# Kernel tuning notes

Hardware: AMD Instinct MI355X
Metric: run time of the kernel (lower is better)

The kernel has to match this reference:

```python
import jax, jax.numpy as jnp
import numpy as np
from jax import lax

NUM_LAYERS = 4
EPS_BN = 1e-5
EPS_AGG = 1e-6


def _bn(x, gamma, beta):
    # training-mode batch norm over the leading (node/edge) dim
    m = x.mean(axis=0)
    v = x.var(axis=0)
    return gamma * (x - m) / jnp.sqrt(v + EPS_BN) + beta


def setup_inputs() -> dict:
    key = jax.random.key(0)
    ks = jax.random.split(key, 32)
    N, E, D, L, K = 50000, 400000, 64, 128, 16
    s = 0.05
    inp = {
        'reads': jax.random.uniform(ks[0], (N, 4, L), jnp.float32),
        'src': jax.random.randint(ks[1], (E,), 0, N, jnp.int32),
        'dst': jax.random.randint(ks[2], (E,), 0, N, jnp.int32),
        'overlap_similarity': jax.random.uniform(ks[3], (E,), jnp.float32),
        'overlap_length': jax.random.normal(ks[4], (E,), jnp.float32),
        # sequence encoder conv: Conv1d(4 -> D, kernel K)
        'conv_w': jax.random.normal(ks[5], (D, 4, K), jnp.float32) * s,
        'conv_b': jnp.zeros((D,), jnp.float32),
        # edge encoder: Linear(2 -> D)
        'We': jax.random.normal(ks[6], (2, D), jnp.float32) * s,
        'be': jnp.zeros((D,), jnp.float32),
        # GatedGCN per-layer weights, stacked on leading layer dim
        'A1': jax.random.normal(ks[7], (NUM_LAYERS, D, D), jnp.float32) * s,
        'A2': jax.random.normal(ks[8], (NUM_LAYERS, D, D), jnp.float32) * s,
        'A3': jax.random.normal(ks[9], (NUM_LAYERS, D, D), jnp.float32) * s,
        'bA1': jnp.zeros((NUM_LAYERS, D), jnp.float32),
        'bA2': jnp.zeros((NUM_LAYERS, D), jnp.float32),
        'bA3': jnp.zeros((NUM_LAYERS, D), jnp.float32),
        'U': jax.random.normal(ks[10], (NUM_LAYERS, D, D), jnp.float32) * s,
        'V': jax.random.normal(ks[11], (NUM_LAYERS, D, D), jnp.float32) * s,
        'bU': jnp.zeros((NUM_LAYERS, D), jnp.float32),
        'bV': jnp.zeros((NUM_LAYERS, D), jnp.float32),
        'bn_h_gamma': jnp.ones((NUM_LAYERS, D), jnp.float32),
        'bn_h_beta': jnp.zeros((NUM_LAYERS, D), jnp.float32),
        'bn_e_gamma': jnp.ones((NUM_LAYERS, D), jnp.float32),
        'bn_e_beta': jnp.zeros((NUM_LAYERS, D), jnp.float32),
        # edge decoder MLP: Linear(3D -> D) -> ReLU -> Linear(D -> 1)
        'W1': jax.random.normal(ks[12], (3 * D, D), jnp.float32) * s,
        'b1': jnp.zeros((D,), jnp.float32),
        'W2': jax.random.normal(ks[13], (D, 1), jnp.float32) * s,
        'b2': jnp.zeros((1,), jnp.float32),
    }
    return inp


def reference(reads, src, dst, overlap_similarity, overlap_length,
              conv_w, conv_b, We, be,
              A1, A2, A3, bA1, bA2, bA3, U, V, bU, bV,
              bn_h_gamma, bn_h_beta, bn_e_gamma, bn_e_beta,
              W1, b1, W2, b2):
    N = reads.shape[0]
    # --- SequenceEncoder: Conv1d over one-hot reads, global max-pool ---
    hseq = lax.conv_general_dilated(
        reads, conv_w, window_strides=(1,), padding='VALID',
        dimension_numbers=('NCH', 'OIH', 'NCH'))  # [N, D, L-K+1]
    h = (hseq + conv_b[None, :, None]).max(axis=2)  # [N, D]
    # --- EdgeEncoder: Linear on [similarity, length] ---
    e = jnp.stack([overlap_similarity, overlap_length], axis=1) @ We + be  # [E, D]
    # --- stacked GatedGCN layers (gather src/dst, scatter-aggregate to dst) ---
    for l in range(NUM_LAYERS):
        hs = h[src]  # [E, D] gather
        hd = h[dst]
        e_hat = (hs @ A1[l] + bA1[l]) + (hd @ A2[l] + bA2[l]) + (e @ A3[l] + bA3[l])
        sigma = jax.nn.sigmoid(e_hat)  # edge gates
        Vh = hs @ V[l] + bV[l]
        num = jax.ops.segment_sum(sigma * Vh, dst, num_segments=N)  # [N, D]
        den = jax.ops.segment_sum(sigma, dst, num_segments=N)
        h_hat = (h @ U[l] + bU[l]) + num / (den + EPS_AGG)
        h = h + jax.nn.relu(_bn(h_hat, bn_h_gamma[l], bn_h_beta[l]))
        e = e + jax.nn.relu(_bn(e_hat, bn_e_gamma[l], bn_e_beta[l]))
    # --- EdgeDecoder: MLP on [h_src, h_dst, e] ---
    z = jnp.concatenate([h[src], h[dst], e], axis=1)  # [E, 3D]
    p = jax.nn.relu(z @ W1 + b1) @ W2 + b2  # [E, 1]
    return p
```

## Files before the change

### kernel.cpp

```cpp
#include <hip/hip_runtime.h>
#include <hip/hip_bf16.h>
#include <cstdint>
#include <cstddef>

#define DD 64

typedef __attribute__((ext_vector_type(8))) short short8;
typedef __attribute__((ext_vector_type(4))) float f32x4;

__device__ __forceinline__ float4 f4_0() { return make_float4(0.f, 0.f, 0.f, 0.f); }

__device__ __forceinline__ unsigned short f2bf(float f) {
  __hip_bfloat16 h = __float2bfloat16(f);
  return *reinterpret_cast<unsigned short*>(&h);
}
__device__ __forceinline__ float bfl(unsigned u) { return __uint_as_float(u << 16); }
__device__ __forceinline__ float bfh(unsigned u) { return __uint_as_float(u & 0xffff0000u); }
__device__ __forceinline__ float b2f(unsigned short u) {
  return __uint_as_float(((unsigned)u) << 16);
}

__device__ __forceinline__ short8 pack_bf16x8(float4 a, float4 b) {
  union { unsigned short us[8]; short8 v; } pk;
  pk.us[0] = f2bf(a.x); pk.us[1] = f2bf(a.y); pk.us[2] = f2bf(a.z); pk.us[3] = f2bf(a.w);
  pk.us[4] = f2bf(b.x); pk.us[5] = f2bf(b.y); pk.us[6] = f2bf(b.z); pk.us[7] = f2bf(b.w);
  return pk.v;
}

__device__ __forceinline__ short8 lds_frag(const unsigned short* p) {
  uint2 lo = *reinterpret_cast<const uint2*>(p);
  uint2 hi = *reinterpret_cast<const uint2*>(p + 4);
  union { unsigned u[4]; short8 v; } t;
  t.u[0] = lo.x; t.u[1] = lo.y; t.u[2] = hi.x; t.u[3] = hi.y;
  return t.v;
}
__device__ __forceinline__ short8 g_frag(const unsigned short* p) {
  return *reinterpret_cast<const short8*>(p);
}

__global__ __launch_bounds__(256) void k_hist(const int* __restrict__ dst,
                                              int* __restrict__ cnt, int E) {
  int j = blockIdx.x * 256 + threadIdx.x;
  if (j < E) atomicAdd(&cnt[dst[j]], 1);
}

__global__ __launch_bounds__(1024) void k_scan(const int* __restrict__ cnt,
                                               int* __restrict__ row_ptr,
                                               int* __restrict__ nxt, int N, int E) {
  __shared__ int wsum[16];
  __shared__ int carry_s;
  const int tid = threadIdx.x;
  const int wid = tid >> 6, lane = tid & 63;
  if (tid == 0) carry_s = 0;
  __syncthreads();
  const int ntl = (N + 4095) / 4096;
  for (int b = 0; b < ntl; ++b) {
    const int i0 = b * 4096 + tid * 4;
    int v0 = 0, v1 = 0, v2 = 0, v3 = 0;
    if (i0 + 3 < N) {
      int4 q = *reinterpret_cast<const int4*>(cnt + i0);
      v0 = q.x; v1 = q.y; v2 = q.z; v3 = q.w;
    } else {
      if (i0 < N) v0 = cnt[i0];
      if (i0 + 1 < N) v1 = cnt[i0 + 1];
      if (i0 + 2 < N) v2 = cnt[i0 + 2];
      if (i0 + 3 < N) v3 = cnt[i0 + 3];
    }
    const int tsum = v0 + v1 + v2 + v3;
    int x = tsum;
#pragma unroll
    for (int off = 1; off < 64; off <<= 1) {
      int y = __shfl_up(x, off, 64);
      if (lane >= off) x += y;
    }
    if (lane == 63) wsum[wid] = x;
    __syncthreads();
    if (wid == 0 && lane < 16) {
      int wv = wsum[lane];
#pragma unroll
      for (int off = 1; off < 16; off <<= 1) {
        int y = __shfl_up(wv, off, 64);
        if (lane >= off) wv += y;
      }
      wsum[lane] = wv;
    }
    __syncthreads();
    int base = carry_s + (wid > 0 ? wsum[wid - 1] : 0) + (x - tsum);
    int e1 = base + v0, e2 = e1 + v1, e3 = e2 + v2;
    if (i0 < N) { row_ptr[i0] = base; nxt[i0] = base; }
    if (i0 + 1 < N) { row_ptr[i0 + 1] = e1; nxt[i0 + 1] = e1; }
    if (i0 + 2 < N) { row_ptr[i0 + 2] = e2; nxt[i0 + 2] = e2; }
    if (i0 + 3 < N) { row_ptr[i0 + 3] = e3; nxt[i0 + 3] = e3; }
    __syncthreads();
    if (tid == 0) carry_s += wsum[15];
    __syncthreads();
  }
  if (tid == 0) row_ptr[N] = E;
}

__global__ __launch_bounds__(256) void k_scatter(const int* __restrict__ dst,
                                                 const int* __restrict__ src,
                                                 int* __restrict__ nxt,
                                                 int* __restrict__ order,
                                                 int* __restrict__ psrc,
                                                 int* __restrict__ pdst, int E) {
  int j = blockIdx.x * 256 + threadIdx.x;
  if (j >= E) return;
  int d = dst[j];
  int pos = atomicAdd(&nxt[d], 1);
  order[pos] = j;
  psrc[pos] = src[j];
  pdst[pos] = d;
}

__global__ __launch_bounds__(256) void k_prep(const float* __restrict__ A1,
                                              const float* __restrict__ A2,
                                              const float* __restrict__ V,
                                              const float* __restrict__ U,
                                              const float* __restrict__ A3,
                                              const float* __restrict__ W1,
                                              unsigned short* __restrict__ T) {
  const int b = blockIdx.x;
  const int tid = threadIdx.x;
  if (b < 20) {
    const int l = b / 5, m = b % 5;
    const float* srcp =
        (m == 0 ? A1 : m == 1 ? A2 : m == 2 ? V : m == 3 ? U : A3) + l * 4096;
    unsigned short* dstp = T + b * 4096;
    for (int i = tid; i < 4096; i += 256) {
      int n = i >> 6, k = i & 63;
      dstp[i] = f2bf(srcp[k * 64 + n]);
    }
  } else {
    unsigned short* dstp = T + 20 * 4096;
    for (int i = tid; i < 12288; i += 256) {
      int n = i / 192, k = i % 192;
      dstp[i] = f2bf(W1[k * 64 + n]);
    }
  }
}

struct ConvRegs { float4 v[3][2]; };

__device__ __forceinline__ void conv_load(const float* __restrict__ reads, int N,
                                          int g, int tid, ConvRegs& R) {
#pragma unroll
  for (int it = 0; it < 3; ++it) {
    const int task = tid + it * 256;
    R.v[it][0] = f4_0(); R.v[it][1] = f4_0();
    if (task < 576) {
      const int node = task / 144, rem = task % 144;
      const int c = rem / 36, u = rem % 36;
      const int gn = g * 4 + node;
      if (gn < N) {
        const float* rp = reads + (size_t)gn * 512 + c * 128 + 4 * u;
        if (u <= 31) R.v[it][0] = *reinterpret_cast<const float4*>(rp);
        if (u <= 30) R.v[it][1] = *reinterpret_cast<const float4*>(rp + 4);
      }
    }
  }
}

__device__ __forceinline__ void conv_write(unsigned short* __restrict__ cbuf,
                                           int tid, const ConvRegs& R) {
#pragma unroll
  for (int it = 0; it < 3; ++it) {
    const int task = tid + it * 256;
    if (task < 576) {
      const int node = task / 144, rem = task % 144;
      const int c = rem / 36, u = rem % 36;
      const float4 v0 = R.v[it][0], v1 = R.v[it][1];
      unsigned pk0, pk1, pk2, pk3;
      asm("v_cvt_pk_bf16_f32 %0, %1, %2" : "=v"(pk0) : "v"(v0.x), "v"(v0.y));
      asm("v_cvt_pk_bf16_f32 %0, %1, %2" : "=v"(pk1) : "v"(v0.z), "v"(v0.w));
      asm("v_cvt_pk_bf16_f32 %0, %1, %2" : "=v"(pk2) : "v"(v1.x), "v"(v1.y));
      asm("v_cvt_pk_bf16_f32 %0, %1, %2" : "=v"(pk3) : "v"(v1.z), "v"(v1.w));
      const unsigned a0 = __builtin_amdgcn_alignbit(pk1, pk0, 16);
      const unsigned a1 = __builtin_amdgcn_alignbit(pk2, pk1, 16);
      const unsigned a2 = __builtin_amdgcn_alignbit(pk3, pk2, 16);
      const int base = ((node * 4 + c) * 4) * 144 + 4 * u;
      *reinterpret_cast<uint2*>(&cbuf[base + 0 * 144]) = make_uint2(pk0, pk1);
      *reinterpret_cast<uint2*>(&cbuf[base + 1 * 144]) = make_uint2(a0, a1);
      *reinterpret_cast<uint2*>(&cbuf[base + 2 * 144]) = make_uint2(pk1, pk2);
      *reinterpret_cast<uint2*>(&cbuf[base + 3 * 144]) = make_uint2(a1, a2);
    }
  }
}

__global__ __launch_bounds__(256) void k_conv_mfma(const float* __restrict__ reads,
                                                   const float* __restrict__ w,
                                                   const float* __restrict__ bias,
                                                   float* __restrict__ h, int N) {
  __shared__ unsigned short cp[2][4 * 4 * 4 * 144];
  const int tid = threadIdx.x;
  const int wid = tid >> 6, lane = tid & 63;
// ... 105 lines not shown
  }
  const int wid = tid >> 6, lane = tid & 63;
  const int col = lane & 15, g = lane >> 4;
  const int ntiles = (N + 15) / 16;
  for (int tw = blockIdx.x * 4 + wid; tw < ntiles; tw += gridDim.x * 4) {
    int n = tw * 16 + col;
    const bool valid = n < N;
    if (!valid) n = N - 1;
    short8 bfr[2];
#pragma unroll
    for (int ks = 0; ks < 2; ++ks) {
      const int c0 = ks * 32 + g * 8;
      const float* hp = h_in + (size_t)n * 64 + c0;
      float4 x0 = *reinterpret_cast<const float4*>(hp);
      float4 x1 = *reinterpret_cast<const float4*>(hp + 4);
      if (hasupd) {
        const float* yp = hhat + (size_t)n * 64 + c0;
        float4 y0 = *reinterpret_cast<const float4*>(yp);
        float4 y1 = *reinterpret_cast<const float4*>(yp + 4);
        float4 sc0 = *reinterpret_cast<const float4*>(&s_coef[c0]);
        float4 sc1 = *reinterpret_cast<const float4*>(&s_coef[c0 + 4]);
        float4 sh0 = *reinterpret_cast<const float4*>(&s_coef[64 + c0]);
        float4 sh1 = *reinterpret_cast<const float4*>(&s_coef[64 + c0 + 4]);
        x0.x += fmaxf(fmaf(sc0.x, y0.x, sh0.x), 0.f);
        x0.y += fmaxf(fmaf(sc0.y, y0.y, sh0.y), 0.f);
        x0.z += fmaxf(fmaf(sc0.z, y0.z, sh0.z), 0.f);
        x0.w += fmaxf(fmaf(sc0.w, y0.w, sh0.w), 0.f);
        x1.x += fmaxf(fmaf(sc1.x, y1.x, sh1.x), 0.f);
        x1.y += fmaxf(fmaf(sc1.y, y1.y, sh1.y), 0.f);
        x1.z += fmaxf(fmaf(sc1.z, y1.z, sh1.z), 0.f);
        x1.w += fmaxf(fmaf(sc1.w, y1.w, sh1.w), 0.f);
        if (valid) {
          float* op = h_out + (size_t)n * 64 + c0;
          *reinterpret_cast<float4*>(op) = x0;
          *reinterpret_cast<float4*>(op + 4) = x1;
        }
      }
      bfr[ks] = pack_bf16x8(x0, x1);
    }
#pragma unroll
    for (int m = 0; m < 4; ++m) {
      const unsigned short* Wm = Wt4 + m * 4096;
      f32x4 acc[4] = {};
#pragma unroll
      for (int ks = 0; ks < 2; ++ks) {
        const int ko = ks * 32 + g * 8;
#pragma unroll
        for (int mt = 0; mt < 4; ++mt) {
          short8 aa = g_frag(Wm + (mt * 16 + col) * 64 + ko);
          acc[mt] = __builtin_amdgcn_mfma_f32_16x16x32_bf16(aa, bfr[ks], acc[mt], 0, 0, 0);
        }
      }
      if (!valid) continue;
      const float* bb = (m == 0) ? bA1 : (m == 1) ? bA2 : (m == 2) ? bV : bU;
#pragma unroll
      for (int mt = 0; mt < 4; ++mt) {
        const int chb = mt * 16 + g * 4;
        float4 bv = *reinterpret_cast<const float4*>(bb + chb);
        float o0 = acc[mt][0] + bv.x;
        float o1 = acc[mt][1] + bv.y;
        float o2 = acc[mt][2] + bv.z;
        float o3 = acc[mt][3] + bv.w;
        if (m < 3) {
          unsigned short* X = (m == 0) ? XA1 : (m == 1) ? XA2 : XV;
          ushort4 ov;
          ov.x = f2bf(o0); ov.y = f2bf(o1); ov.z = f2bf(o2); ov.w = f2bf(o3);
          *reinterpret_cast<ushort4*>(X + (size_t)n * 64 + chb) = ov;
        } else {
          *reinterpret_cast<float4*>(XU + (size_t)n * 64 + chb) =
              make_float4(o0, o1, o2, o3);
        }
      }
    }
  }
}

__global__ __launch_bounds__(256) void k_edge_mfma0(unsigned short* __restrict__ e,
                                                    unsigned short* __restrict__ ehat_out,
                                                    const float* __restrict__ sim,
                                                    const float* __restrict__ olen,
                                                    const int* __restrict__ order,
                                                    const float* __restrict__ We,
                                                    const float* __restrict__ be,
                                                    const int* __restrict__ psrc,
                                                    const int* __restrict__ pdst,
                                                    const unsigned short* __restrict__ XA1,
                                                    const unsigned short* __restrict__ XA2,
                                                    const unsigned short* __restrict__ A3t,
                                                    const float* __restrict__ bA3,
                                                    float* __restrict__ sums_out, int E) {
  __shared__ float s_sums[128];
  const int tid = threadIdx.x;
  if (tid < 128) s_sums[tid] = 0.f;
  __syncthreads();
  const int wid = tid >> 6, lane = tid & 63;
  const int col = lane & 15, g = lane >> 4;
  short8 aa[4][2];
#pragma unroll
  for (int mt = 0; mt < 4; ++mt)
#pragma unroll
    for (int ks = 0; ks < 2; ++ks)
      aa[mt][ks] = g_frag(A3t + (mt * 16 + col) * 64 + ks * 32 + g * 8);
  float4 ba[4];
#pragma unroll
  for (int mt = 0; mt < 4; ++mt)
    ba[mt] = *reinterpret_cast<const float4*>(bA3 + mt * 16 + g * 4);
  float4 w0[2][2], w1[2][2], bev[2][2];
#pragma unroll
  for (int ks = 0; ks < 2; ++ks) {
    const int c0 = ks * 32 + g * 8;
    w0[ks][0] = *reinterpret_cast<const float4*>(We + c0);
    w0[ks][1] = *reinterpret_cast<const float4*>(We + c0 + 4);
    w1[ks][0] = *reinterpret_cast<const float4*>(We + 64 + c0);
    w1[ks][1] = *reinterpret_cast<const float4*>(We + 64 + c0 + 4);
    bev[ks][0] = *reinterpret_cast<const float4*>(be + c0);
    bev[ks][1] = *reinterpret_cast<const float4*>(be + c0 + 4);
  }
  float statS[16], statQ[16];
#pragma unroll
  for (int i = 0; i < 16; ++i) { statS[i] = 0.f; statQ[i] = 0.f; }
  const int ntiles = (E + 15) / 16;
  for (int tw = blockIdx.x * 4 + wid; tw < ntiles; tw += gridDim.x * 4) {
    int p = tw * 16 + col;
    const bool valid = p < E;
    if (!valid) p = E - 1;
    const int se = psrc[p], de = pdst[p];
    const int oe = order[p];
    const float sv = sim[oe], lv = olen[oe];
    short8 bfr[2];
#pragma unroll
    for (int ks = 0; ks < 2; ++ks) {
      float4 e0, e1;
      e0.x = fmaf(sv, w0[ks][0].x, fmaf(lv, w1[ks][0].x, bev[ks][0].x));
      e0.y = fmaf(sv, w0[ks][0].y, fmaf(lv, w1[ks][0].y, bev[ks][0].y));
      e0.z = fmaf(sv, w0[ks][0].z, fmaf(lv, w1[ks][0].z, bev[ks][0].z));
      e0.w = fmaf(sv, w0[ks][0].w, fmaf(lv, w1[ks][0].w, bev[ks][0].w));
      e1.x = fmaf(sv, w0[ks][1].x, fmaf(lv, w1[ks][1].x, bev[ks][1].x));
      e1.y = fmaf(sv, w0[ks][1].y, fmaf(lv, w1[ks][1].y, bev[ks][1].y));
      e1.z = fmaf(sv, w0[ks][1].z, fmaf(lv, w1[ks][1].z, bev[ks][1].z));
      e1.w = fmaf(sv, w0[ks][1].w, fmaf(lv, w1[ks][1].w, bev[ks][1].w));
      bfr[ks] = pack_bf16x8(e0, e1);
      if (valid)
        *reinterpret_cast<short8*>(e + (size_t)p * 64 + ks * 32 + g * 8) = bfr[ks];
    }
    f32x4 acc[4] = {};
#pragma unroll
    for (int ks = 0; ks < 2; ++ks)
#pragma unroll
      for (int mt = 0; mt < 4; ++mt)
        acc[mt] = __builtin_amdgcn_mfma_f32_16x16x32_bf16(aa[mt][ks], bfr[ks], acc[mt], 0, 0, 0);
    if (valid) {
#pragma unroll
      for (int mt = 0; mt < 4; ++mt) {
        const int chb = mt * 16 + g * 4;
        ushort4 x1 = *reinterpret_cast<const ushort4*>(XA1 + (size_t)se * 64 + chb);
        ushort4 x2 = *reinterpret_cast<const ushort4*>(XA2 + (size_t)de * 64 + chb);
        float o0 = acc[mt][0] + b2f(x1.x) + b2f(x2.x) + ba[mt].x;
        float o1 = acc[mt][1] + b2f(x1.y) + b2f(x2.y) + ba[mt].y;
        float o2 = acc[mt][2] + b2f(x1.z) + b2f(x2.z) + ba[mt].z;
        float o3 = acc[mt][3] + b2f(x1.w) + b2f(x2.w) + ba[mt].w;
        ushort4 ov;
        ov.x = f2bf(o0); ov.y = f2bf(o1); ov.z = f2bf(o2); ov.w = f2bf(o3);
        *reinterpret_cast<ushort4*>(ehat_out + (size_t)p * 64 + chb) = ov;
        statS[mt * 4 + 0] += o0; statQ[mt * 4 + 0] = fmaf(o0, o0, statQ[mt * 4 + 0]);
        statS[mt * 4 + 1] += o1; statQ[mt * 4 + 1] = fmaf(o1, o1, statQ[mt * 4 + 1]);
        statS[mt * 4 + 2] += o2; statQ[mt * 4 + 2] = fmaf(o2, o2, statQ[mt * 4 + 2]);
        statS[mt * 4 + 3] += o3; statQ[mt * 4 + 3] = fmaf(o3, o3, statQ[mt * 4 + 3]);
      }
    }
  }
#pragma unroll
  for (int off = 1; off <= 8; off <<= 1)
#pragma unroll
    for (int i = 0; i < 16; ++i) {
      statS[i] += __shfl_xor(statS[i], off, 64);
      statQ[i] += __shfl_xor(statQ[i], off, 64);
    }
  if (col == 0) {
#pragma unroll
    for (int mt = 0; mt < 4; ++mt)
#pragma unroll
      for (int c = 0; c < 4; ++c) {
        const int ch = mt * 16 + g * 4 + c;
        atomicAdd(&s_sums[ch], statS[mt * 4 + c]);
        atomicAdd(&s_sums[64 + ch], statQ[mt * 4 + c]);
      }
  }
  __syncthreads();
  if (tid < 128) atomicAdd(&sums_out[tid], s_sums[tid]);
}

__global__ __launch_bounds__(256) void k_edge_mfma(unsigned short* __restrict__ e,
                                                   const unsigned short* __restrict__ ehat_prev,
                                                   unsigned short* __restrict__ ehat_out,
                                                   const float* __restrict__ sums_prev,
                                                   const float* __restrict__ gprev,
                                                   const float* __restrict__ bprev,
                                                   const int* __restrict__ psrc,
                                                   const int* __restrict__ pdst,
                                                   const unsigned short* __restrict__ XA1,
                                                   const unsigned short* __restrict__ XA2,
                                                   const unsigned short* __restrict__ A3t,
                                                   const float* __restrict__ bA3,
                                                   float* __restrict__ sums_out, int E) {
  __shared__ float s_coef[128];
  __shared__ float s_sums[128];
  const int tid = threadIdx.x;
  if (tid < 128) s_sums[tid] = 0.f;
  if (tid < 64) {
    float mean = sums_prev[tid] / (float)E;
    float var = sums_prev[64 + tid] / (float)E - mean * mean;
    float sc = gprev[tid] * rsqrtf(var + 1e-5f);
    s_coef[tid] = sc;
    s_coef[64 + tid] = bprev[tid] - mean * sc;
  }
  __syncthreads();
  const int wid = tid >> 6, lane = tid & 63;
  const int col = lane & 15, g = lane >> 4;
  short8 aa[4][2];
#pragma unroll
  for (int mt = 0; mt < 4; ++mt)
#pragma unroll
    for (int ks = 0; ks < 2; ++ks)
      aa[mt][ks] = g_frag(A3t + (mt * 16 + col) * 64 + ks * 32 + g * 8);
  float4 ba[4];
#pragma unroll
  for (int mt = 0; mt < 4; ++mt)
    ba[mt] = *reinterpret_cast<const float4*>(bA3 + mt * 16 + g * 4);
  float statS[16], statQ[16];
#pragma unroll
  for (int i = 0; i < 16; ++i) { statS[i] = 0.f; statQ[i] = 0.f; }
  const int ntiles = (E + 15) / 16;
  for (int tw = blockIdx.x * 4 + wid; tw < ntiles; tw += gridDim.x * 4) {
    int p = tw * 16 + col;
    const bool valid = p < E;
    if (!valid) p = E - 1;
    const int se = psrc[p], de = pdst[p];
    short8 bfr[2];
#pragma unroll
    for (int ks = 0; ks < 2; ++ks) {
      const int c0 = ks * 32 + g * 8;
      uint4 eo = *reinterpret_cast<const uint4*>(e + (size_t)p * 64 + c0);
      float4 e0 = make_float4(bfl(eo.x), bfh(eo.x), bfl(eo.y), bfh(eo.y));
      float4 e1 = make_float4(bfl(eo.z), bfh(eo.z), bfl(eo.w), bfh(eo.w));
      uint4 hv = *reinterpret_cast<const uint4*>(ehat_prev + (size_t)p * 64 + c0);
      float4 sc0 = *reinterpret_cast<const float4*>(&s_coef[c0]);
      float4 sc1 = *reinterpret_cast<const float4*>(&s_coef[c0 + 4]);
      float4 sh0 = *reinterpret_cast<const float4*>(&s_coef[64 + c0]);
      float4 sh1 = *reinterpret_cast<const float4*>(&s_coef[64 + c0 + 4]);
      e0.x += fmaxf(fmaf(sc0.x, bfl(hv.x), sh0.x), 0.f);
      e0.y += fmaxf(fmaf(sc0.y, bfh(hv.x), sh0.y), 0.f);
      e0.z += fmaxf(fmaf(sc0.z, bfl(hv.y), sh0.z), 0.f);
      e0.w += fmaxf(fmaf(sc0.w, bfh(hv.y), sh0.w), 0.f);
      e1.x += fmaxf(fmaf(sc1.x, bfl(hv.z), sh1.x), 0.f);
      e1.y += fmaxf(fmaf(sc1.y, bfh(hv.z), sh1.y), 0.f);
      e1.z += fmaxf(fmaf(sc1.z, bfl(hv.w), sh1.z), 0.f);
      e1.w += fmaxf(fmaf(sc1.w, bfh(hv.w), sh1.w), 0.f);
      bfr[ks] = pack_bf16x8(e0, e1);
      if (valid)
        *reinterpret_cast<short8*>(e + (size_t)p * 64 + c0) = bfr[ks];
    }
    f32x4 acc[4] = {};
#pragma unroll
    for (int ks = 0; ks < 2; ++ks)
#pragma unroll
      for (int mt = 0; mt < 4; ++mt)
        acc[mt] = __builtin_amdgcn_mfma_f32_16x16x32_bf16(aa[mt][ks], bfr[ks], acc[mt], 0, 0, 0);
    if (valid) {
#pragma unroll
      for (int mt = 0; mt < 4; ++mt) {
        const int chb = mt * 16 + g * 4;
        ushort4 x1 = *reinterpret_cast<const ushort4*>(XA1 + (size_t)se * 64 + chb);
        ushort4 x2 = *reinterpret_cast<const ushort4*>(XA2 + (size_t)de * 64 + chb);
        float o0 = acc[mt][0] + b2f(x1.x) + b2f(x2.x) + ba[mt].x;
        float o1 = acc[mt][1] + b2f(x1.y) + b2f(x2.y) + ba[mt].y;
        float o2 = acc[mt][2] + b2f(x1.z) + b2f(x2.z) + ba[mt].z;
        float o3 = acc[mt][3] + b2f(x1.w) + b2f(x2.w) + ba[mt].w;
        ushort4 ov;
        ov.x = f2bf(o0); ov.y = f2bf(o1); ov.z = f2bf(o2); ov.w = f2bf(o3);
        *reinterpret_cast<ushort4*>(ehat_out + (size_t)p * 64 + chb) = ov;
        statS[mt * 4 + 0] += o0; statQ[mt * 4 + 0] = fmaf(o0, o0, statQ[mt * 4 + 0]);
        statS[mt * 4 + 1] += o1; statQ[mt * 4 + 1] = fmaf(o1, o1, statQ[mt * 4 + 1]);
        statS[mt * 4 + 2] += o2; statQ[mt * 4 + 2] = fmaf(o2, o2, statQ[mt * 4 + 2]);
        statS[mt * 4 + 3] += o3; statQ[mt * 4 + 3] = fmaf(o3, o3, statQ[mt * 4 + 3]);
      }
    }
  }
#pragma unroll
  for (int off = 1; off <= 8; off <<= 1)
#pragma unroll
    for (int i = 0; i < 16; ++i) {
      statS[i] += __shfl_xor(statS[i], off, 64);
      statQ[i] += __shfl_xor(statQ[i], off, 64);
    }
  if (col == 0) {
#pragma unroll
    for (int mt = 0; mt < 4; ++mt)
#pragma unroll
      for (int c = 0; c < 4; ++c) {
        const int ch = mt * 16 + g * 4 + c;
        atomicAdd(&s_sums[ch], statS[mt * 4 + c]);
        atomicAdd(&s_sums[64 + ch], statQ[mt * 4 + c]);
      }
  }
  __syncthreads();
  if (tid < 128) atomicAdd(&sums_out[tid], s_sums[tid]);
}

__global__ __launch_bounds__(256) void k_agg(const int* __restrict__ row_ptr,
                                             const int* __restrict__ psrc,
                                             const unsigned short* __restrict__ ehat,
                                             const unsigned short* __restrict__ XV,
                                             const float* __restrict__ XU,
                                             float* __restrict__ hhat,
                                             float* __restrict__ sums_h, int N) {
  __shared__ float s_sums[128];
  const int tid = threadIdx.x;
  if (tid < 128) s_sums[tid] = 0.f;
  __syncthreads();
  float sS[4] = {0.f, 0.f, 0.f, 0.f}, sQ[4] = {0.f, 0.f, 0.f, 0.f};
  const int total = N * 16;
  for (int idx = blockIdx.x * 256 + tid; idx < total; idx += gridDim.x * 256) {
    int n = idx >> 4, dc = (idx & 15) << 2;
    int beg = row_ptr[n], end = row_ptr[n + 1];
    float4 nm = f4_0(), dn = f4_0();
    for (int i = beg; i < end; ++i) {
      int sj = psrc[i];
      uint2 ev = *reinterpret_cast<const uint2*>(ehat + (size_t)i * 64 + dc);
      uint2 vv = *reinterpret_cast<const uint2*>(XV + (size_t)sj * 64 + dc);
      float s0 = 1.f / (1.f + __expf(-bfl(ev.x)));
      float s1 = 1.f / (1.f + __expf(-bfh(ev.x)));
      float s2 = 1.f / (1.f + __expf(-bfl(ev.y)));
      float s3 = 1.f / (1.f + __expf(-bfh(ev.y)));
      dn.x += s0; dn.y += s1; dn.z += s2; dn.w += s3;
      nm.x = fmaf(s0, bfl(vv.x), nm.x);
      nm.y = fmaf(s1, bfh(vv.x), nm.y);
      nm.z = fmaf(s2, bfl(vv.y), nm.z);
      nm.w = fmaf(s3, bfh(vv.y), nm.w);
    }
    float4 xu = *reinterpret_cast<const float4*>(XU + (size_t)n * 64 + dc);
    float h0 = xu.x + nm.x / (dn.x + 1e-6f);
    float h1 = xu.y + nm.y / (dn.y + 1e-6f);
    float h2 = xu.z + nm.z / (dn.z + 1e-6f);
    float h3 = xu.w + nm.w / (dn.w + 1e-6f);
    *reinterpret_cast<float4*>(hhat + (size_t)n * 64 + dc) = make_float4(h0, h1, h2, h3);
    sS[0] += h0; sQ[0] = fmaf(h0, h0, sQ[0]);
    sS[1] += h1; sQ[1] = fmaf(h1, h1, sQ[1]);
    sS[2] += h2; sQ[2] = fmaf(h2, h2, sQ[2]);
    sS[3] += h3; sQ[3] = fmaf(h3, h3, sQ[3]);
  }
#pragma unroll
  for (int off = 16; off <= 32; off <<= 1)
#pragma unroll
    for (int c = 0; c < 4; ++c) {
      sS[c] += __shfl_xor(sS[c], off, 64);
      sQ[c] += __shfl_xor(sQ[c], off, 64);
    }
  const int lane = tid & 63;
  if (lane < 16) {
    const int dc = lane << 2;
#pragma unroll
    for (int c = 0; c < 4; ++c) {
      atomicAdd(&s_sums[dc + c], sS[c]);
      atomicAdd(&s_sums[64 + dc + c], sQ[c]);
    }
  }
  __syncthreads();
  if (tid < 128) atomicAdd(&sums_h[tid], s_sums[tid]);
}

__global__ __launch_bounds__(256) void k_update_h(float* __restrict__ h,
                                                  const float* __restrict__ hhat,
                                                  const float* __restrict__ sums,
                                                  const float* __restrict__ gamma,
                                                  const float* __restrict__ beta, int R) {
  int idx = blockIdx.x * 256 + threadIdx.x;
  if (idx >= R * 16) return;
  int r = idx >> 4, dc = (idx & 15) << 2;
  const float invR = 1.f / (float)R;
  float4 sv = *reinterpret_cast<const float4*>(sums + dc);
  float4 qv = *reinterpret_cast<const float4*>(sums + 64 + dc);
  float4 gm = *reinterpret_cast<const float4*>(gamma + dc);
  float4 bt = *reinterpret_cast<const float4*>(beta + dc);
  float m0 = sv.x * invR, m1 = sv.y * invR, m2 = sv.z * invR, m3 = sv.w * invR;
  float c0 = gm.x * rsqrtf(qv.x * invR - m0 * m0 + 1e-5f);
  float c1 = gm.y * rsqrtf(qv.y * invR - m1 * m1 + 1e-5f);
  float c2 = gm.z * rsqrtf(qv.z * invR - m2 * m2 + 1e-5f);
  float c3 = gm.w * rsqrtf(qv.w * invR - m3 * m3 + 1e-5f);
  float h0 = bt.x - m0 * c0, h1 = bt.y - m1 * c1, h2 = bt.z - m2 * c2, h3 = bt.w - m3 * c3;
  size_t off = (size_t)r * 64 + dc;
  float4 y = *reinterpret_cast<const float4*>(hhat + off);
  float4 x = *reinterpret_cast<const float4*>(h + off);
  x.x += fmaxf(fmaf(c0, y.x, h0), 0.f);
  x.y += fmaxf(fmaf(c1, y.y, h1), 0.f);
  x.z += fmaxf(fmaf(c2, y.z, h2), 0.f);
  x.w += fmaxf(fmaf(c3, y.w, h3), 0.f);
  *reinterpret_cast<float4*>(h + off) = x;
}

__global__ __launch_bounds__(256) void k_decoder_mfma(const float* __restrict__ h,
                                                      const unsigned short* __restrict__ e,
                                                      const unsigned short* __restrict__ ehat3,
                                                      const float* __restrict__ sums_e3,
                                                      const float* __restrict__ ge3,
                                                      const float* __restrict__ be3,
                                                      const int* __restrict__ psrc,
                                                      const int* __restrict__ pdst,
                                                      const int* __restrict__ order,
                                                      const unsigned short* __restrict__ W1t,
                                                      const float* __restrict__ b1,
                                                      const float* __restrict__ W2,
                                                      const float* __restrict__ b2,
                                                      float* __restrict__ out, int E) {
  __shared__ unsigned short Wt[64 * 200];
  __shared__ float s_coef[128];
  const int tid = threadIdx.x;
  if (tid < 64) {
    float mean = sums_e3[tid] / (float)E;
    float var = sums_e3[64 + tid] / (float)E - mean * mean;
    float sc = ge3[tid] * rsqrtf(var + 1e-5f);
    s_coef[tid] = sc;
    s_coef[64 + tid] = be3[tid] - mean * sc;
  }
  for (int i = tid; i < 1536; i += 256) {
    int n = i / 24, kc = (i % 24) * 8;
    *reinterpret_cast<uint4*>(&Wt[n * 200 + kc]) =
        *reinterpret_cast<const uint4*>(W1t + n * 192 + kc);
  }
  __syncthreads();
  const int wid = tid >> 6, lane = tid & 63;
  const int col = lane & 15, g = lane >> 4;
  float b1v[4], w2v[4];
#pragma unroll
  for (int nt = 0; nt < 4; ++nt) { b1v[nt] = b1[nt * 16 + col]; w2v[nt] = W2[nt * 16 + col]; }
  const float bb2 = b2[0];
  const int ntiles = (E + 15) / 16;
  for (int tw = blockIdx.x * 4 + wid; tw < ntiles; tw += gridDim.x * 4) {
    const int eb = tw * 16;
    int p = eb + col;
    if (p >= E) p = E - 1;
    const int se = psrc[p], de = pdst[p];
    f32x4 acc[4] = {};
#pragma unroll
    for (int ks = 0; ks < 6; ++ks) {
      float4 a0, a1;
      if (ks < 4) {
        const float* ap = (ks < 2 ? h + (size_t)se * 64 : h + (size_t)de * 64) + (ks & 1) * 32 + g * 8;
        a0 = *reinterpret_cast<const float4*>(ap);
        a1 = *reinterpret_cast<const float4*>(ap + 4);
      } else {
        const int c0 = (ks - 4) * 32 + g * 8;
        uint4 eo = *reinterpret_cast<const uint4*>(e + (size_t)p * 64 + c0);
        a0 = make_float4(bfl(eo.x), bfh(eo.x), bfl(eo.y), bfh(eo.y));
        a1 = make_float4(bfl(eo.z), bfh(eo.z), bfl(eo.w), bfh(eo.w));
        uint4 hv = *reinterpret_cast<const uint4*>(ehat3 + (size_t)p * 64 + c0);
        float4 sc0 = *reinterpret_cast<const float4*>(&s_coef[c0]);
        float4 sc1 = *reinterpret_cast<const float4*>(&s_coef[c0 + 4]);
        float4 sh0 = *reinterpret_cast<const float4*>(&s_coef[64 + c0]);
        float4 sh1 = *reinterpret_cast<const float4*>(&s_coef[64 + c0 + 4]);
        a0.x += fmaxf(fmaf(sc0.x, bfl(hv.x), sh0.x), 0.f);
        a0.y += fmaxf(fmaf(sc0.y, bfh(hv.x), sh0.y), 0.f);
        a0.z += fmaxf(fmaf(sc0.z, bfl(hv.y), sh0.z), 0.f);
        a0.w += fmaxf(fmaf(sc0.w, bfh(hv.y), sh0.w), 0.f);
        a1.x += fmaxf(fmaf(sc1.x, bfl(hv.z), sh1.x), 0.f);
        a1.y += fmaxf(fmaf(sc1.y, bfh(hv.z), sh1.y), 0.f);
        a1.z += fmaxf(fmaf(sc1.z, bfl(hv.w), sh1.z), 0.f);
        a1.w += fmaxf(fmaf(sc1.w, bfh(hv.w), sh1.w), 0.f);
      }
      short8 af = pack_bf16x8(a0, a1);
#pragma unroll
      for (int nt = 0; nt < 4; ++nt) {
        short8 bb = lds_frag(&Wt[(nt * 16 + col) * 200 + ks * 32 + g * 8]);
        acc[nt] = __builtin_amdgcn_mfma_f32_16x16x32_bf16(af, bb, acc[nt], 0, 0, 0);
      }
    }
    float pr[4];
#pragma unroll
    for (int r = 0; r < 4; ++r) {
      float s = 0.f;
#pragma unroll
      for (int nt = 0; nt < 4; ++nt)
        s = fmaf(fmaxf(acc[nt][r] + b1v[nt], 0.f), w2v[nt], s);
      pr[r] = s;
    }
#pragma unroll
    for (int off = 1; off <= 8; off <<= 1)
#pragma unroll
      for (int r = 0; r < 4; ++r)
        pr[r] += __shfl_xor(pr[r], off, 64);
    if (col == 0) {
#pragma unroll
      for (int r = 0; r < 4; ++r) {
        int m = eb + g * 4 + r;
        if (m < E) out[order[m]] = pr[r] + bb2;
      }
    }
  }
}

extern "C" void kernel_launch(void* const* d_in, const int* in_sizes, int n_in,
                              void* d_out, int out_size, void* d_ws, size_t ws_size,
                              hipStream_t stream) {
  const float* reads  = (const float*)d_in[0];
  const int*   src    = (const int*)d_in[1];
  const int*   dst    = (const int*)d_in[2];
  const float* sim    = (const float*)d_in[3];
  const float* olen   = (const float*)d_in[4];
  const float* conv_w = (const float*)d_in[5];
  const float* conv_b = (const float*)d_in[6];
  const float* We     = (const float*)d_in[7];
  const float* be     = (const float*)d_in[8];
  const float* A1     = (const float*)d_in[9];
  const float* A2     = (const float*)d_in[10];
  const float* A3     = (const float*)d_in[11];
  const float* bA1    = (const float*)d_in[12];
  const float* bA2    = (const float*)d_in[13];
  const float* bA3    = (const float*)d_in[14];
  const float* U      = (const float*)d_in[15];
  const float* V      = (const float*)d_in[16];
  const float* bU     = (const float*)d_in[17];
  const float* bV     = (const float*)d_in[18];
  const float* bnhg   = (const float*)d_in[19];
  const float* bnhb   = (const float*)d_in[20];
  const float* bneg   = (const float*)d_in[21];
  const float* bneb   = (const float*)d_in[22];
  const float* W1     = (const float*)d_in[23];
  const float* b1     = (const float*)d_in[24];
  const float* W2     = (const float*)d_in[25];
  const float* b2     = (const float*)d_in[26];

  const int N = in_sizes[0] / 512;
  const int E = in_sizes[1];

  float* fp = (float*)d_ws;
  float* hA   = fp; fp += (size_t)N * 64;
  float* hB   = fp; fp += (size_t)N * 64;
  float* hhat = fp; fp += (size_t)N * 64;
  float* XU   = fp; fp += (size_t)N * 64;
  float* sums = fp; fp += 1024;
  unsigned short* up = (unsigned short*)fp;
  unsigned short* e     = up; up += (size_t)E * 64;
  unsigned short* ehatA = up; up += (size_t)E * 64;
  unsigned short* ehatB = up; up += (size_t)E * 64;
  unsigned short* XA1 = up; up += (size_t)N * 64;
  unsigned short* XA2 = up; up += (size_t)N * 64;
  unsigned short* XV  = up; up += (size_t)N * 64;
  unsigned short* Wt  = up; up += 20 * 4096 + 12288;
  int* ip = (int*)up;
  int* order   = ip; ip += E;
  int* psrc    = ip; ip += E;
  int* pdst    = ip; ip += E;
  int* cnt     = ip; ip += N;
  int* nxt     = ip; ip += N;
  int* row_ptr = ip; ip += N + 1;
  float* out = (float*)d_out;

  hipMemsetAsync(cnt, 0, sizeof(int) * N, stream);
  hipMemsetAsync(sums, 0, sizeof(float) * 1024, stream);
  k_hist<<<(E + 255) / 256, 256, 0, stream>>>(dst, cnt, E);
  k_prep<<<21, 256, 0, stream>>>(A1, A2, V, U, A3, W1, Wt);
  k_scan<<<1, 1024, 0, stream>>>(cnt, row_ptr, nxt, N, E);
  k_scatter<<<(E + 255) / 256, 256, 0, stream>>>(dst, src, nxt, order, psrc, pdst, E);

  const int ngroups = (N + 3) / 4;
  const int CG = ngroups < 1024 ? ngroups : 1024;
  k_conv_mfma<<<CG, 256, 0, stream>>>(reads, conv_w, conv_b, hA, N);

  const int EPBLK = 2048;
  const int APBLK = 1024;
  const int NPB = 512;
  float* hin = hA;
  float* hout = hB;
  unsigned short* ehat_cur = ehatA;
  unsigned short* ehat_prev = ehatB;
  for (int l = 0; l < 4; ++l) {
    ehat_cur = (l & 1) ? ehatB : ehatA;
    ehat_prev = (l & 1) ? ehatA : ehatB;
    float* sums_e = sums + l * 128;
    float* sums_h = sums + 512 + l * 128;
    k_node_mfma<<<NPB, 256, 0, stream>>>(
        hin, (l > 0) ? hout : nullptr, hhat,
        (l > 0) ? (sums + 512 + (l - 1) * 128) : sums,
        bnhg + (l > 0 ? (l - 1) * 64 : 0), bnhb + (l > 0 ? (l - 1) * 64 : 0),
        Wt + l * 5 * 4096,
        bA1 + l * 64, bA2 + l * 64, bV + l * 64, bU + l * 64,
        XA1, XA2, XV, XU, N, l > 0 ? 1 : 0);
    if (l > 0) { float* t = hin; hin = hout; hout = t; }
    if (l == 0) {
      k_edge_mfma0<<<EPBLK, 256, 0, stream>>>(
          e, ehat_cur, sim, olen, order, We, be, psrc, pdst, XA1, XA2,
          Wt + 4 * 4096, bA3, sums_e, E);
    } else {
      k_edge_mfma<<<EPBLK, 256, 0, stream>>>(
          e, ehat_prev, ehat_cur, sums + (l - 1) * 128,
          bneg + (l - 1) * 64, bneb + (l - 1) * 64,
          psrc, pdst, XA1, XA2, Wt + (l * 5 + 4) * 4096, bA3 + l * 64, sums_e, E);
    }
    k_agg<<<APBLK, 256, 0, stream>>>(row_ptr, psrc, ehat_cur, XV, XU, hhat, sums_h, N);
  }

  k_update_h<<<(N * 16 + 255) / 256, 256, 0, stream>>>(
      hin, hhat, sums + 512 + 3 * 128, bnhg + 3 * 64, bnhb + 3 * 64, N);
  k_decoder_mfma<<<EPBLK, 256, 0, stream>>>(
      hin, e, ehat_cur, sums + 3 * 128, bneg + 3 * 64, bneb + 3 * 64,
      psrc, pdst, order, Wt + 20 * 4096, b1, W2, b2, out, E);
}
```

Measured before the change: 856.0 us.

## Prefetch next-tile edge data, pack src/dst pairs, bf16 decoder node features

The edge kernels now software-pipeline their grid-stride loop. Each iteration prefetches the next tile's packed (src,dst) int2 indices and its contiguous e/ehat rows, and issues the XA1/XA2 gathers before the MFMA so their latency overlaps compute. The A3 weight fragments are reloaded from global memory inside the loop instead of being held in registers, which frees registers for the prefetched data. The final h update also writes a bf16 copy of h, so the decoder gathers half the bytes and skips the float-to-bf16 packing for node features. The edge grid is halved to 1024 blocks, which lowers occupancy in exchange for longer per-wave loops and more register room.

```diff
diff --git a/kernel.cpp b/kernel.cpp
--- a/kernel.cpp
+++ b/kernel.cpp
@@ -36,6 +36,9 @@
 }
 __device__ __forceinline__ short8 g_frag(const unsigned short* p) {
   return *reinterpret_cast<const short8*>(p);
+}
+__device__ __forceinline__ short8 u4_to_s8(uint4 v) {
+  union { uint4 u; short8 s; } t; t.u = v; return t.s;
 }
 
 __global__ __launch_bounds__(256) void k_hist(const int* __restrict__ dst,
@@ -103,14 +106,15 @@
                                                  int* __restrict__ nxt,
                                                  int* __restrict__ order,
                                                  int* __restrict__ psrc,
-                                                 int* __restrict__ pdst, int E) {
+                                                 int2* __restrict__ pedge, int E) {
   int j = blockIdx.x * 256 + threadIdx.x;
   if (j >= E) return;
   int d = dst[j];
+  int s = src[j];
   int pos = atomicAdd(&nxt[d], 1);
   order[pos] = j;
-  psrc[pos] = src[j];
-  pdst[pos] = d;
+  psrc[pos] = s;
+  pedge[pos] = make_int2(s, d);
 }
 
 __global__ __launch_bounds__(256) void k_prep(const float* __restrict__ A1,
@@ -382,8 +386,7 @@
                                                     const int* __restrict__ order,
                                                     const float* __restrict__ We,
                                                     const float* __restrict__ be,
-                                                    const int* __restrict__ psrc,
-                                                    const int* __restrict__ pdst,
+                                                    const int2* __restrict__ pedge,
                                                     const unsigned short* __restrict__ XA1,
                                                     const unsigned short* __restrict__ XA2,
                                                     const unsigned short* __restrict__ A3t,
@@ -395,12 +398,6 @@
   __syncthreads();
   const int wid = tid >> 6, lane = tid & 63;
   const int col = lane & 15, g = lane >> 4;
-  short8 aa[4][2];
-#pragma unroll
-  for (int mt = 0; mt < 4; ++mt)
-#pragma unroll
-    for (int ks = 0; ks < 2; ++ks)
-      aa[mt][ks] = g_frag(A3t + (mt * 16 + col) * 64 + ks * 32 + g * 8);
   float4 ba[4];
 #pragma unroll
   for (int mt = 0; mt < 4; ++mt)
@@ -420,13 +417,34 @@
 #pragma unroll
   for (int i = 0; i < 16; ++i) { statS[i] = 0.f; statQ[i] = 0.f; }
   const int ntiles = (E + 15) / 16;
-  for (int tw = blockIdx.x * 4 + wid; tw < ntiles; tw += gridDim.x * 4) {
+  const int stride = gridDim.x * 4;
+  int tw = blockIdx.x * 4 + wid;
+  int2 idx_n = make_int2(0, 0);
+  int oe_n = 0;
+  if (tw < ntiles) {
+    int p = tw * 16 + col; if (p >= E) p = E - 1;
+    idx_n = pedge[p];
+    oe_n = order[p];
+  }
+  for (; tw < ntiles; tw += stride) {
     int p = tw * 16 + col;
     const bool valid = p < E;
     if (!valid) p = E - 1;
-    const int se = psrc[p], de = pdst[p];
-    const int oe = order[p];
-    const float sv = sim[oe], lv = olen[oe];
+    const int se = idx_n.x, de = idx_n.y;
+    const float sv = sim[oe_n], lv = olen[oe_n];
+    ushort4 gx1[4], gx2[4];
+#pragma unroll
+    for (int mt = 0; mt < 4; ++mt) {
+      const int chb = mt * 16 + g * 4;
+      gx1[mt] = *reinterpret_cast<const ushort4*>(XA1 + (size_t)se * 64 + chb);
+      gx2[mt] = *reinterpret_cast<const ushort4*>(XA2 + (size_t)de * 64 + chb);
+    }
+    const int twn = tw + stride;
+    if (twn < ntiles) {
+      int pn = twn * 16 + col; if (pn >= E) pn = E - 1;
+      idx_n = pedge[pn];
+      oe_n = order[pn];
+    }
     short8 bfr[2];
 #pragma unroll
     for (int ks = 0; ks < 2; ++ks) {
@@ -447,18 +465,18 @@
 #pragma unroll
     for (int ks = 0; ks < 2; ++ks)
 #pragma unroll
-      for (int mt = 0; mt < 4; ++mt)
-        acc[mt] = __builtin_amdgcn_mfma_f32_16x16x32_bf16(aa[mt][ks], bfr[ks], acc[mt], 0, 0, 0);
+      for (int mt = 0; mt < 4; ++mt) {
+        short8 aa = g_frag(A3t + (mt * 16 + col) * 64 + ks * 32 + g * 8);
+        acc[mt] = __builtin_amdgcn_mfma_f32_16x16x32_bf16(aa, bfr[ks], acc[mt], 0, 0, 0);
+      }
     if (valid) {
 #pragma unroll
       for (int mt = 0; mt < 4; ++mt) {
         const int chb = mt * 16 + g * 4;
-        ushort4 x1 = *reinterpret_cast<const ushort4*>(XA1 + (size_t)se * 64 + chb);
-        ushort4 x2 = *reinterpret_cast<const ushort4*>(XA2 + (size_t)de * 64 + chb);
-        float o0 = acc[mt][0] + b2f(x1.x) + b2f(x2.x) + ba[mt].x;
-        float o1 = acc[mt][1] + b2f(x1.y) + b2f(x2.y) + ba[mt].y;
-        float o2 = acc[mt][2] + b2f(x1.z) + b2f(x2.z) + ba[mt].z;
-        float o3 = acc[mt][3] + b2f(x1.w) + b2f(x2.w) + ba[mt].w;
+        float o0 = acc[mt][0] + b2f(gx1[mt].x) + b2f(gx2[mt].x) + ba[mt].x;
+        float o1 = acc[mt][1] + b2f(gx1[mt].y) + b2f(gx2[mt].y) + ba[mt].y;
+        float o2 = acc[mt][2] + b2f(gx1[mt].z) + b2f(gx2[mt].z) + ba[mt].z;
+        float o3 = acc[mt][3] + b2f(gx1[mt].w) + b2f(gx2[mt].w) + ba[mt].w;
         ushort4 ov;
         ov.x = f2bf(o0); ov.y = f2bf(o1); ov.z = f2bf(o2); ov.w = f2bf(o3);
         *reinterpret_cast<ushort4*>(ehat_out + (size_t)p * 64 + chb) = ov;
@@ -496,8 +514,7 @@
                                                    const float* __restrict__ sums_prev,
                                                    const float* __restrict__ gprev,
                                                    const float* __restrict__ bprev,
-                                                   const int* __restrict__ psrc,
-                                                   const int* __restrict__ pdst,
+                                                   const int2* __restrict__ pedge,
                                                    const unsigned short* __restrict__ XA1,
                                                    const unsigned short* __restrict__ XA2,
                                                    const unsigned short* __restrict__ A3t,
@@ -517,12 +534,6 @@
   __syncthreads();
   const int wid = tid >> 6, lane = tid & 63;
   const int col = lane & 15, g = lane >> 4;
-  short8 aa[4][2];
-#pragma unroll
-  for (int mt = 0; mt < 4; ++mt)
-#pragma unroll
-    for (int ks = 0; ks < 2; ++ks)
-      aa[mt][ks] = g_frag(A3t + (mt * 16 + col) * 64 + ks * 32 + g * 8);
   float4 ba[4];
 #pragma unroll
   for (int mt = 0; mt < 4; ++mt)
@@ -531,19 +542,53 @@
 #pragma unroll
   for (int i = 0; i < 16; ++i) { statS[i] = 0.f; statQ[i] = 0.f; }
   const int ntiles = (E + 15) / 16;
-  for (int tw = blockIdx.x * 4 + wid; tw < ntiles; tw += gridDim.x * 4) {
+  const int stride = gridDim.x * 4;
+  int tw = blockIdx.x * 4 + wid;
+  int2 idx_n = make_int2(0, 0);
+  uint4 eo_n0, eo_n1, hv_n0, hv_n1;
+  if (tw < ntiles) {
+    int p = tw * 16 + col; if (p >= E) p = E - 1;
+    idx_n = pedge[p];
+    const unsigned short* ep = e + (size_t)p * 64 + g * 8;
+    eo_n0 = *reinterpret_cast<const uint4*>(ep);
+    eo_n1 = *reinterpret_cast<const uint4*>(ep + 32);
+    const unsigned short* hp = ehat_prev + (size_t)p * 64 + g * 8;
+    hv_n0 = *reinterpret_cast<const uint4*>(hp);
+    hv_n1 = *reinterpret_cast<const uint4*>(hp + 32);
+  }
+  for (; tw < ntiles; tw += stride) {
     int p = tw * 16 + col;
     const bool valid = p < E;
     if (!valid) p = E - 1;
-    const int se = psrc[p], de = pdst[p];
+    const int se = idx_n.x, de = idx_n.y;
+    const uint4 eoc[2] = {eo_n0, eo_n1};
+    const uint4 hvc[2] = {hv_n0, hv_n1};
+    ushort4 gx1[4], gx2[4];
+#pragma unroll
+    for (int mt = 0; mt < 4; ++mt) {
+      const int chb = mt * 16 + g * 4;
+      gx1[mt] = *reinterpret_cast<const ushort4*>(XA1 + (size_t)se * 64 + chb);
+      gx2[mt] = *reinterpret_cast<const ushort4*>(XA2 + (size_t)de * 64 + chb);
+    }
+    const int twn = tw + stride;
+    if (twn < ntiles) {
+      int pn = twn * 16 + col; if (pn >= E) pn = E - 1;
+      idx_n = pedge[pn];
+      const unsigned short* ep = e + (size_t)pn * 64 + g * 8;
+      eo_n0 = *reinterpret_cast<const uint4*>(ep);
+      eo_n1 = *reinterpret_cast<const uint4*>(ep + 32);
+      const unsigned short* hp = ehat_prev + (size_t)pn * 64 + g * 8;
+      hv_n0 = *reinterpret_cast<const uint4*>(hp);
+      hv_n1 = *reinterpret_cast<const uint4*>(hp + 32);
+    }
     short8 bfr[2];
 #pragma unroll
     for (int ks = 0; ks < 2; ++ks) {
       const int c0 = ks * 32 + g * 8;
-      uint4 eo = *reinterpret_cast<const uint4*>(e + (size_t)p * 64 + c0);
+      const uint4 eo = eoc[ks];
+      const uint4 hv = hvc[ks];
       float4 e0 = make_float4(bfl(eo.x), bfh(eo.x), bfl(eo.y), bfh(eo.y));
       float4 e1 = make_float4(bfl(eo.z), bfh(eo.z), bfl(eo.w), bfh(eo.w));
-      uint4 hv = *reinterpret_cast<const uint4*>(ehat_prev + (size_t)p * 64 + c0);
       float4 sc0 = *reinterpret_cast<const float4*>(&s_coef[c0]);
       float4 sc1 = *reinterpret_cast<const float4*>(&s_coef[c0 + 4]);
       float4 sh0 = *reinterpret_cast<const float4*>(&s_coef[64 + c0]);
@@ -564,18 +609,18 @@
 #pragma unroll
     for (int ks = 0; ks < 2; ++ks)
 #pragma unroll
-      for (int mt = 0; mt < 4; ++mt)
-        acc[mt] = __builtin_amdgcn_mfma_f32_16x16x32_bf16(aa[mt][ks], bfr[ks], acc[mt], 0, 0, 0);
+      for (int mt = 0; mt < 4; ++mt) {
+        short8 aa = g_frag(A3t + (mt * 16 + col) * 64 + ks * 32 + g * 8);
+        acc[mt] = __builtin_amdgcn_mfma_f32_16x16x32_bf16(aa, bfr[ks], acc[mt], 0, 0, 0);
+      }
     if (valid) {
 #pragma unroll
       for (int mt = 0; mt < 4; ++mt) {
         const int chb = mt * 16 + g * 4;
-        ushort4 x1 = *reinterpret_cast<const ushort4*>(XA1 + (size_t)se * 64 + chb);
-        ushort4 x2 = *reinterpret_cast<const ushort4*>(XA2 + (size_t)de * 64 + chb);
-        float o0 = acc[mt][0] + b2f(x1.x) + b2f(x2.x) + ba[mt].x;
-        float o1 = acc[mt][1] + b2f(x1.y) + b2f(x2.y) + ba[mt].y;
-        float o2 = acc[mt][2] + b2f(x1.z) + b2f(x2.z) + ba[mt].z;
-        float o3 = acc[mt][3] + b2f(x1.w) + b2f(x2.w) + ba[mt].w;
+        float o0 = acc[mt][0] + b2f(gx1[mt].x) + b2f(gx2[mt].x) + ba[mt].x;
+        float o1 = acc[mt][1] + b2f(gx1[mt].y) + b2f(gx2[mt].y) + ba[mt].y;
+        float o2 = acc[mt][2] + b2f(gx1[mt].z) + b2f(gx2[mt].z) + ba[mt].z;
+        float o3 = acc[mt][3] + b2f(gx1[mt].w) + b2f(gx2[mt].w) + ba[mt].w;
         ushort4 ov;
         ov.x = f2bf(o0); ov.y = f2bf(o1); ov.z = f2bf(o2); ov.w = f2bf(o3);
         *reinterpret_cast<ushort4*>(ehat_out + (size_t)p * 64 + chb) = ov;
@@ -670,6 +715,7 @@
 }
 
 __global__ __launch_bounds__(256) void k_update_h(float* __restrict__ h,
+                                                  unsigned short* __restrict__ hb,
                                                   const float* __restrict__ hhat,
                                                   const float* __restrict__ sums,
                                                   const float* __restrict__ gamma,
@@ -696,16 +742,18 @@
   x.z += fmaxf(fmaf(c2, y.z, h2), 0.f);
   x.w += fmaxf(fmaf(c3, y.w, h3), 0.f);
   *reinterpret_cast<float4*>(h + off) = x;
-}
-
-__global__ __launch_bounds__(256) void k_decoder_mfma(const float* __restrict__ h,
+  ushort4 hv;
+  hv.x = f2bf(x.x); hv.y = f2bf(x.y); hv.z = f2bf(x.z); hv.w = f2bf(x.w);
+  *reinterpret_cast<ushort4*>(hb + off) = hv;
+}
+
+__global__ __launch_bounds__(256) void k_decoder_mfma(const unsigned short* __restrict__ hb,
                                                       const unsigned short* __restrict__ e,
                                                       const unsigned short* __restrict__ ehat3,
                                                       const float* __restrict__ sums_e3,
                                                       const float* __restrict__ ge3,
                                                       const float* __restrict__ be3,
-                                                      const int* __restrict__ psrc,
-                                                      const int* __restrict__ pdst,
+                                                      const int2* __restrict__ pedge,
                                                       const int* __restrict__ order,
                                                       const unsigned short* __restrict__ W1t,
                                                       const float* __restrict__ b1,
@@ -735,25 +783,58 @@
   for (int nt = 0; nt < 4; ++nt) { b1v[nt] = b1[nt * 16 + col]; w2v[nt] = W2[nt * 16 + col]; }
   const float bb2 = b2[0];
   const int ntiles = (E + 15) / 16;
-  for (int tw = blockIdx.x * 4 + wid; tw < ntiles; tw += gridDim.x * 4) {
+  const int stride = gridDim.x * 4;
+  int tw = blockIdx.x * 4 + wid;
+  int2 idx_n = make_int2(0, 0);
+  uint4 eo_n0, eo_n1, hv_n0, hv_n1;
+  if (tw < ntiles) {
+    int p = tw * 16 + col; if (p >= E) p = E - 1;
+    idx_n = pedge[p];
+    const unsigned short* ep = e + (size_t)p * 64 + g * 8;
+    eo_n0 = *reinterpret_cast<const uint4*>(ep);
+    eo_n1 = *reinterpret_cast<const uint4*>(ep + 32);
+    const unsigned short* hp = ehat3 + (size_t)p * 64 + g * 8;
+    hv_n0 = *reinterpret_cast<const uint4*>(hp);
+    hv_n1 = *reinterpret_cast<const uint4*>(hp + 32);
+  }
+  for (; tw < ntiles; tw += stride) {
     const int eb = tw * 16;
     int p = eb + col;
-    if (p >= E) p = E - 1;
-    const int se = psrc[p], de = pdst[p];
+    const bool valid = p < E;
+    if (!valid) p = E - 1;
+    const int se = idx_n.x, de = idx_n.y;
+    const uint4 eoc[2] = {eo_n0, eo_n1};
+    const uint4 hvc[2] = {hv_n0, hv_n1};
+    short8 haf[4];
+#pragma unroll
+    for (int ks = 0; ks < 4; ++ks) {
+      const unsigned short* hp = hb + (size_t)(ks < 2 ? se : de) * 64 + (ks & 1) * 32 + g * 8;
+      haf[ks] = g_frag(hp);
+    }
+    const int twn = tw + stride;
+    if (twn < ntiles) {
+      int pn = twn * 16 + col; if (pn >= E) pn = E - 1;
+      idx_n = pedge[pn];
+      const unsigned short* ep = e + (size_t)pn * 64 + g * 8;
+      eo_n0 = *reinterpret_cast<const uint4*>(ep);
+      eo_n1 = *reinterpret_cast<const uint4*>(ep + 32);
+      const unsigned short* hp = ehat3 + (size_t)pn * 64 + g * 8;
+      hv_n0 = *reinterpret_cast<const uint4*>(hp);
+      hv_n1 = *reinterpret_cast<const uint4*>(hp + 32);
+    }
     f32x4 acc[4] = {};
 #pragma unroll
     for (int ks = 0; ks < 6; ++ks) {
-      float4 a0, a1;
+      short8 af;
       if (ks < 4) {
-        const float* ap = (ks < 2 ? h + (size_t)se * 64 : h + (size_t)de * 64) + (ks & 1) * 32 + g * 8;
-        a0 = *reinterpret_cast<const float4*>(ap);
-        a1 = *reinterpret_cast<const float4*>(ap + 4);
+        af = haf[ks];
       } else {
-        const int c0 = (ks - 4) * 32 + g * 8;
-        uint4 eo = *reinterpret_cast<const uint4*>(e + (size_t)p * 64 + c0);
-        a0 = make_float4(bfl(eo.x), bfh(eo.x), bfl(eo.y), bfh(eo.y));
-        a1 = make_float4(bfl(eo.z), bfh(eo.z), bfl(eo.w), bfh(eo.w));
-        uint4 hv = *reinterpret_cast<const uint4*>(ehat3 + (size_t)p * 64 + c0);
+        const int kse = ks - 4;
+        const int c0 = kse * 32 + g * 8;
+        const uint4 eo = eoc[kse];
+        const uint4 hv = hvc[kse];
+        float4 a0 = make_float4(bfl(eo.x), bfh(eo.x), bfl(eo.y), bfh(eo.y));
+        float4 a1 = make_float4(bfl(eo.z), bfh(eo.z), bfl(eo.w), bfh(eo.w));
         float4 sc0 = *reinterpret_cast<const float4*>(&s_coef[c0]);
         float4 sc1 = *reinterpret_cast<const float4*>(&s_coef[c0 + 4]);
         float4 sh0 = *reinterpret_cast<const float4*>(&s_coef[64 + c0]);
@@ -766,8 +847,8 @@
         a1.y += fmaxf(fmaf(sc1.y, bfh(hv.z), sh1.y), 0.f);
         a1.z += fmaxf(fmaf(sc1.z, bfl(hv.w), sh1.z), 0.f);
         a1.w += fmaxf(fmaf(sc1.w, bfh(hv.w), sh1.w), 0.f);
-      }
-      short8 af = pack_bf16x8(a0, a1);
+        af = pack_bf16x8(a0, a1);
+      }
 #pragma unroll
       for (int nt = 0; nt < 4; ++nt) {
         short8 bb = lds_frag(&Wt[(nt * 16 + col) * 200 + ks * 32 + g * 8]);
@@ -845,11 +926,12 @@
   unsigned short* XA1 = up; up += (size_t)N * 64;
   unsigned short* XA2 = up; up += (size_t)N * 64;
   unsigned short* XV  = up; up += (size_t)N * 64;
+  unsigned short* hb  = up; up += (size_t)N * 64;
   unsigned short* Wt  = up; up += 20 * 4096 + 12288;
   int* ip = (int*)up;
   int* order   = ip; ip += E;
   int* psrc    = ip; ip += E;
-  int* pdst    = ip; ip += E;
+  int2* pedge  = (int2*)ip; ip += 2 * (size_t)E;
   int* cnt     = ip; ip += N;
   int* nxt     = ip; ip += N;
   int* row_ptr = ip; ip += N + 1;
@@ -860,13 +942,13 @@
   k_hist<<<(E + 255) / 256, 256, 0, stream>>>(dst, cnt, E);
   k_prep<<<21, 256, 0, stream>>>(A1, A2, V, U, A3, W1, Wt);
   k_scan<<<1, 1024, 0, stream>>>(cnt, row_ptr, nxt, N, E);
-  k_scatter<<<(E + 255) / 256, 256, 0, stream>>>(dst, src, nxt, order, psrc, pdst, E);
+  k_scatter<<<(E + 255) / 256, 256, 0, stream>>>(dst, src, nxt, order, psrc, pedge, E);
 
   const int ngroups = (N + 3) / 4;
   const int CG = ngroups < 1024 ? ngroups : 1024;
   k_conv_mfma<<<CG, 256, 0, stream>>>(reads, conv_w, conv_b, hA, N);
 
-  const int EPBLK = 2048;
+  const int EPBLK = 1024;
   const int APBLK = 1024;
   const int NPB = 512;
   float* hin = hA;
@@ -888,20 +970,20 @@
     if (l > 0) { float* t = hin; hin = hout; hout = t; }
     if (l == 0) {
       k_edge_mfma0<<<EPBLK, 256, 0, stream>>>(
-          e, ehat_cur, sim, olen, order, We, be, psrc, pdst, XA1, XA2,
+          e, ehat_cur, sim, olen, order, We, be, pedge, XA1, XA2,
           Wt + 4 * 4096, bA3, sums_e, E);
     } else {
       k_edge_mfma<<<EPBLK, 256, 0, stream>>>(
           e, ehat_prev, ehat_cur, sums + (l - 1) * 128,
           bneg + (l - 1) * 64, bneb + (l - 1) * 64,
-          psrc, pdst, XA1, XA2, Wt + (l * 5 + 4) * 4096, bA3 + l * 64, sums_e, E);
+          pedge, XA1, XA2, Wt + (l * 5 + 4) * 4096, bA3 + l * 64, sums_e, E);
     }
     k_agg<<<APBLK, 256, 0, stream>>>(row_ptr, psrc, ehat_cur, XV, XU, hhat, sums_h, N);
   }
 
   k_update_h<<<(N * 16 + 255) / 256, 256, 0, stream>>>(
-      hin, hhat, sums + 512 + 3 * 128, bnhg + 3 * 64, bnhb + 3 * 64, N);
+      hin, hb, hhat, sums + 512 + 3 * 128, bnhg + 3 * 64, bnhb + 3 * 64, N);
   k_decoder_mfma<<<EPBLK, 256, 0, stream>>>(
-      hin, e, ehat_cur, sums + 3 * 128, bneg + 3 * 64, bneb + 3 * 64,
-      psrc, pdst, order, Wt + 20 * 4096, b1, W2, b2, out, E);
-}
+      hb, e, ehat_cur, sums + 3 * 128, bneg + 3 * 64, bneb + 3 * 64,
+      pedge, order, Wt + 20 * 4096, b1, W2, b2, out, E);
+}
```

Result: faster. 768.6 us (-10.2%).
